# Optimization experiments

Measured on AMD Instinct MI355X. Metric: run time of the kernel, lower is better.

Reference implementation:

```python
import jax, jax.numpy as jnp
import numpy as np

B, S, R = 8, 4096, 512
E, K, ATOMS, XAR, TOPK = 64, 256, 16, 3, 2
TEMP = 1.0


def setup_inputs() -> dict:
    key = jax.random.key(0)
    k0, k1, k2, k3, k4 = jax.random.split(key, 5)
    x_latent = jax.random.normal(k0, (B, S, R), jnp.float32)
    router_w = jax.random.normal(k1, (E, R), jnp.float32) * (1.0 / np.sqrt(R))
    atoms = jax.random.normal(k2, (E, ATOMS, R), jnp.float32) * 0.01
    combo_weights = jax.random.uniform(k3, (E, K, XAR), jnp.float32) * 0.5 + 0.25
    combo_logits = jax.random.normal(k4, (E, K, XAR, ATOMS), jnp.float32) * 0.01
    return {"x_latent": x_latent, "router_w": router_w, "atoms": atoms,
            "combo_weights": combo_weights, "combo_logits": combo_logits}


def _expert_centroids(atoms, combo_weights, combo_logits):
    # Hard codeword path (vectorized over experts):
    # sign atoms -> pick argmax atom per (k, xor slot) -> weight -> sum -> sign -> mean over k
    binary = jnp.sign(atoms)                                   # [E, A, R]
    # softmax(logits/t) then argmax == argmax(logits) (monotone)
    idx = jnp.argmax(combo_logits, axis=-1)                    # [E, K, XAR]
    sel = binary[jnp.arange(E)[:, None, None], idx]            # [E, K, XAR, R]
    codewords = jnp.sign((sel * combo_weights[..., None]).sum(axis=2))  # [E, K, R]
    return codewords.mean(axis=1)                              # [E, R]


def reference(x_latent, router_w, atoms, combo_weights, combo_logits):
    t = max(TEMP, 0.1)
    router_logits = jnp.einsum('bsr,er->bse', x_latent, router_w)   # [B, S, E]
    probs_t = jax.nn.softmax(router_logits / t, axis=-1)
    gates, expert_ids = jax.lax.top_k(probs_t, TOPK)                # [B, S, 2]
    gates = gates / gates.sum(axis=-1, keepdims=True)

    centroids = _expert_centroids(atoms, combo_weights, combo_logits)  # [E, R]

    # aux load-balancing loss (uses untempered softmax)
    router_prob = jax.nn.softmax(router_logits, axis=-1)
    aux_loss = E * jnp.sum(router_prob.mean(axis=(0, 1)) *
                           (router_prob > 0).astype(x_latent.dtype).mean(axis=(0, 1)))

    # dense per-expert gate = sum over topk slots of gate * (id == e), then combine with centroids
    dense_gates = (jax.nn.one_hot(expert_ids, E, dtype=gates.dtype) *
                   gates[..., None]).sum(axis=-2)                    # [B, S, E]
    combined = jnp.einsum('bse,er->bsr', dense_gates, centroids)     # [B, S, R]
    return combined, aux_loss
```

## Files before the change

### kernel.cpp

```cpp
#include <hip/hip_runtime.h>
#include <math.h>

#define TOKENS 32768
#define RDIM 512
#define NEXP 64
#define NK 256
#define LDB 264
#define PSTR 67
#define TAU 4.0e-3f

typedef unsigned short u16;
typedef float f32x4 __attribute__((ext_vector_type(4)));
typedef short s16x8 __attribute__((ext_vector_type(8)));

#define MFMA_B16(a, b, c) __builtin_amdgcn_mfma_f32_16x16x32_bf16(a, b, c, 0, 0, 0)

__device__ __forceinline__ void split_pack(float4 v, unsigned& h01, unsigned& h23,
                                           unsigned& l01, unsigned& l23) {
    unsigned u0 = __float_as_uint(v.x), u1 = __float_as_uint(v.y);
    unsigned u2 = __float_as_uint(v.z), u3 = __float_as_uint(v.w);
    float r0 = v.x - __uint_as_float(u0 & 0xFFFF0000u);
    float r1 = v.y - __uint_as_float(u1 & 0xFFFF0000u);
    float r2 = v.z - __uint_as_float(u2 & 0xFFFF0000u);
    float r3 = v.w - __uint_as_float(u3 & 0xFFFF0000u);
    h01 = (u0 >> 16) | (u1 & 0xFFFF0000u);
    h23 = (u2 >> 16) | (u3 & 0xFFFF0000u);
    l01 = (__float_as_uint(r0) >> 16) | (__float_as_uint(r1) & 0xFFFF0000u);
    l23 = (__float_as_uint(r2) >> 16) | (__float_as_uint(r3) & 0xFFFF0000u);
}

__device__ __forceinline__ void split8(float4 a, float4 b, s16x8& hi, s16x8& lo) {
    union U { unsigned u[4]; s16x8 v; };
    U H, L;
    split_pack(a, H.u[0], H.u[1], L.u[0], L.u[1]);
    split_pack(b, H.u[2], H.u[3], L.u[2], L.u[3]);
    hi = H.v; lo = L.v;
}

__global__ __launch_bounds__(256) void centroid_kernel(
    const float* __restrict__ atoms,
    const float* __restrict__ cw,
    const float* __restrict__ cl,
    float* __restrict__ cent,
    float* __restrict__ aux_sum,
    unsigned* __restrict__ aux_cnt,
    unsigned* __restrict__ done)
{
    __shared__ unsigned pack[NK];
    const int e    = blockIdx.x >> 1;
    const int half = blockIdx.x & 1;
    const int tid  = threadIdx.x;

    if (blockIdx.x == 0 && tid < 64) { aux_sum[tid] = 0.f; aux_cnt[tid] = 0u; }
    if (done && blockIdx.x == 0 && tid == 0) *done = 0u;

    {
        const int k = tid;
        unsigned u = 0;
        float w3[3];
        #pragma unroll
        for (int xx = 0; xx < 3; ++xx) {
            const float* cp = cl + ((((size_t)e * NK + k) * 3 + xx) << 4);
            float v[16];
            *(float4*)(v + 0)  = *(const float4*)(cp + 0);
            *(float4*)(v + 4)  = *(const float4*)(cp + 4);
            *(float4*)(v + 8)  = *(const float4*)(cp + 8);
            *(float4*)(v + 12) = *(const float4*)(cp + 12);
            float best = v[0]; int bi = 0;
            #pragma unroll
            for (int a = 1; a < 16; ++a) {
                if (v[a] > best) { best = v[a]; bi = a; }
            }
            u |= (unsigned)bi << (4 * xx);
            w3[xx] = cw[((size_t)e * NK + k) * 3 + xx];
        }
        unsigned lut = 0;
        #pragma unroll
        for (int c = 0; c < 8; ++c) {
            float val = ((c & 1) ? -w3[0] : w3[0])
                      + ((c & 2) ? -w3[1] : w3[1])
                      + ((c & 4) ? -w3[2] : w3[2]);
            lut |= (val < 0.f ? 1u : 0u) << c;
        }
        pack[k] = u | (lut << 16);
    }

    const int r = half * 256 + tid;
    unsigned B0 = 0;
    #pragma unroll
    for (int a = 0; a < 16; ++a)
        B0 |= (atoms[((size_t)e * 16 + a) * RDIM + r] < 0.f ? 1u : 0u) << a;
    __syncthreads();

    int n0 = 0;
    for (int k = 0; k < NK; ++k) {
        unsigned u  = pack[k];
        unsigned i0 = u & 15u, i1 = (u >> 4) & 15u, i2 = (u >> 8) & 15u;
        unsigned c0 = ((B0 >> i0) & 1u) | (((B0 >> i1) & 1u) << 1) | (((B0 >> i2) & 1u) << 2);
        n0 += (u >> (16 + c0)) & 1u;
    }
    cent[(size_t)e * RDIM + r] = 1.f - (float)n0 * (1.f / 128.f);
}

__global__ __launch_bounds__(512, 2) void moe_main(
    const float* __restrict__ x,
    const float* __restrict__ w,
    const float* __restrict__ cent,
    float* __restrict__ out,
    float* __restrict__ aux_sum,
    unsigned* __restrict__ aux_cnt,
    unsigned* __restrict__ done,
    float* __restrict__ out_aux,
    int fuse)
{
    __shared__ u16 wlds[2 * 64 * LDB];
    u16* whi = wlds;
    u16* wlo = wlds + 64 * LDB;
    float* P     = (float*)wlds;
    float* candv = P + 128 * PSTR;
    int*   candi = (int*)(candv + 128 * 13);
    float* qsum  = (float*)(candi + 128 * 13);
    float* gateL = qsum + 128 * 5;
    __shared__ float s_aux[64];
    __shared__ unsigned s_cnt[64];
    __shared__ int s_last;

    const int tid  = threadIdx.x;
    const int lane = tid & 63;
    const int wave = tid >> 6;
    const int l15  = lane & 15;
    const int kgrp = (lane >> 4) << 3;
    const int tok0 = blockIdx.x * 128;

    if (tid < 64) { s_aux[tid] = 0.f; s_cnt[tid] = 0u; }

    f32x4 acc[4];
    #pragma unroll
    for (int nt = 0; nt < 4; ++nt) acc[nt] = (f32x4){0.f, 0.f, 0.f, 0.f};

    const float* xlane = x + (size_t)(tok0 + wave * 16 + l15) * RDIM + kgrp;
    const int wrow = tid >> 3;
    const int wseg = tid & 7;
    const float* wg = w + (size_t)wrow * RDIM + wseg * 32;
    const int woff = wrow * LDB + wseg * 32;

    float4 wpre[8];
    #pragma unroll
    for (int j = 0; j < 8; ++j) wpre[j] = *(const float4*)(wg + j * 4);

    float4 preA[4], preB[4];
    #pragma unroll
    for (int i = 0; i < 4; ++i) {
        preA[i] = *(const float4*)(xlane + i * 32);
        preB[i] = *(const float4*)(xlane + i * 32 + 4);
    }

    #pragma unroll
    for (int h = 0; h < 2; ++h) {
        if (h) __syncthreads();
        #pragma unroll
        for (int j = 0; j < 8; ++j) {
            unsigned h01, h23, l01, l23;
            split_pack(wpre[j], h01, h23, l01, l23);
            *(uint2*)&whi[woff + j * 4] = make_uint2(h01, h23);
            *(uint2*)&wlo[woff + j * 4] = make_uint2(l01, l23);
        }
        __syncthreads();

        #pragma unroll
        for (int kb = 0; kb < 8; ++kb) {
            s16x8 ah, al;
            split8(preA[kb & 3], preB[kb & 3], ah, al);
            const int gk = h * 8 + kb + 4;
            if (gk < 16) {
                const float* nx = xlane + gk * 32;
                preA[kb & 3] = *(const float4*)(nx);
                preB[kb & 3] = *(const float4*)(nx + 4);
            }
            if (h == 0 && kb == 2) {
                #pragma unroll
                for (int j = 0; j < 8; ++j)
                    wpre[j] = *(const float4*)(wg + 256 + j * 4);
            }
            const int kl = kb * 32 + kgrp;
            #pragma unroll
            for (int nt = 0; nt < 4; ++nt) {
                const int brow = nt * 16 + l15;
                s16x8 bh = *(const s16x8*)&whi[brow * LDB + kl];
                s16x8 bl = *(const s16x8*)&wlo[brow * LDB + kl];
                acc[nt] = MFMA_B16(ah, bh, acc[nt]);
                acc[nt] = MFMA_B16(ah, bl, acc[nt]);
                acc[nt] = MFMA_B16(al, bh, acc[nt]);
            }
        }
    }

    __syncthreads();
    #pragma unroll
    for (int nt = 0; nt < 4; ++nt)
        #pragma unroll
        for (int i = 0; i < 4; ++i)
            P[(wave * 16 + ((lane >> 4) << 2) + i) * PSTR + nt * 16 + l15] = acc[nt][i];
    __syncthreads();

    const int tt = tid & 127;
    const int ss = tid >> 7;
    float v[16];
    #pragma unroll
    for (int j = 0; j < 16; ++j) v[j] = P[tt * PSTR + ss * 16 + j];

    float m1 = -INFINITY, m2 = -INFINITY, m3 = -INFINITY;
    int   i1 = NEXP, i2 = NEXP, i3 = NEXP;
    #pragma unroll
    for (int j = 0; j < 16; ++j) {
        float val = v[j]; int e = ss * 16 + j;
        if (val > m1)      { m3 = m2; i3 = i2; m2 = m1; i2 = i1; m1 = val; i1 = e; }
        else if (val > m2) { m3 = m2; i3 = i2; m2 = val; i2 = e; }
        else if (val > m3) { m3 = val; i3 = e; }
    }
    candv[tt * 13 + ss * 3 + 0] = m1; candi[tt * 13 + ss * 3 + 0] = i1;
    candv[tt * 13 + ss * 3 + 1] = m2; candi[tt * 13 + ss * 3 + 1] = i2;
    candv[tt * 13 + ss * 3 + 2] = m3; candi[tt * 13 + ss * 3 + 2] = i3;
    __syncthreads();

    m1 = m2 = m3 = -INFINITY; i1 = i2 = i3 = NEXP;
    #pragma unroll
    for (int q = 0; q < 12; ++q) {
        float val = candv[tt * 13 + q]; int e = candi[tt * 13 + q];
        if (val > m1)      { m3 = m2; i3 = i2; m2 = m1; i2 = i1; m1 = val; i1 = e; }
        else if (val > m2) { m3 = m2; i3 = i2; m2 = val; i2 = e; }
        else if (val > m3) { m3 = val; i3 = e; }
    }

    float ex[16]; float ps = 0.f;
    #pragma unroll
    for (int j = 0; j < 16; ++j) { ex[j] = __expf(v[j] - m1); ps += ex[j]; }
    qsum[tt * 5 + ss] = ps;

    if (ss == 0) {
        {
            const float ed  = __expf(m2 - m1);
            const float inv = 1.f / (1.f + ed);
            gateL[tt * 4 + 0] = inv;
            gateL[tt * 4 + 1] = ed * inv;
            ((int*)gateL)[tt * 4 + 2] = i1;
            ((int*)gateL)[tt * 4 + 3] = i2;
        }
        const int tbase = wave << 6;
        unsigned long long bmask = __ballot(m2 - m3 < TAU);
        while (bmask) {
            const int f = __ffsll(bmask) - 1;
            bmask &= bmask - 1;
            int id3[3];
            id3[0] = __shfl(i1, f); id3[1] = __shfl(i2, f); id3[2] = __shfl(i3, f);
            const float* xrow = x + (size_t)(tok0 + tbase + f) * RDIM + lane * 8;
            float4 a0 = *(const float4*)(xrow);
            float4 a1 = *(const float4*)(xrow + 4);
            float d[3];
            #pragma unroll
            for (int jj = 0; jj < 3; ++jj) {
                const float* wrow = w + (size_t)id3[jj] * RDIM + lane * 8;
                float4 b0 = *(const float4*)(wrow);
                float4 b1 = *(const float4*)(wrow + 4);
                float p = a0.x * b0.x;
                p = fmaf(a0.y, b0.y, p); p = fmaf(a0.z, b0.z, p); p = fmaf(a0.w, b0.w, p);
                p = fmaf(a1.x, b1.x, p); p = fmaf(a1.y, b1.y, p);
                p = fmaf(a1.z, b1.z, p); p = fmaf(a1.w, b1.w, p);
                #pragma unroll
                for (int off = 32; off; off >>= 1) p += __shfl_xor(p, off);
                d[jj] = p;
            }
            int b = 0;
            if (d[1] > d[0] || (d[1] == d[0] && id3[1] < id3[0])) b = 1;
            if (d[2] > d[b] || (d[2] == d[b] && id3[2] < id3[b])) b = 2;
            int sec;
            if (b == 0)      sec = (d[1] > d[2] || (d[1] == d[2] && id3[1] < id3[2])) ? 1 : 2;
            else if (b == 1) sec = (d[0] > d[2] || (d[0] == d[2] && id3[0] < id3[2])) ? 0 : 2;
            else             sec = (d[0] > d[1] || (d[0] == d[1] && id3[0] < id3[1])) ? 0 : 1;
            if (lane == f) {
                const float ed  = __expf(d[sec] - d[b]);
                const float inv = 1.f / (1.f + ed);
                gateL[(tbase + f) * 4 + 0] = inv;
                gateL[(tbase + f) * 4 + 1] = ed * inv;
                ((int*)gateL)[(tbase + f) * 4 + 2] = id3[b];
                ((int*)gateL)[(tbase + f) * 4 + 3] = id3[sec];
            }
        }
    }
    __syncthreads();

    float Z = 0.f;
    #pragma unroll
    for (int k = 0; k < 4; ++k) Z += qsum[tt * 5 + k];
    const float invZ = 1.f / Z;
    #pragma unroll
    for (int j = 0; j < 16; ++j) P[tt * PSTR + ss * 16 + j] = ex[j] * invZ;
    __syncthreads();

    {
        const int e = tid & 63, tq = tid >> 6;
        float s = 0.f; unsigned cn = 0u;
        #pragma unroll
        for (int t = 0; t < 16; ++t) {
            float pv = P[(tq * 16 + t) * PSTR + e];
            s += pv; cn += (pv > 0.f) ? 1u : 0u;
        }
        atomicAdd(&s_aux[e], s);
        atomicAdd(&s_cnt[e], cn);
    }
    __syncthreads();
    if (tid < 64) {
        atomicAdd(aux_sum + tid, s_aux[tid]);
        atomicAdd(aux_cnt + tid, s_cnt[tid]);
    }

    {
        const int e = lane;
        #pragma unroll
        for (int s2 = 0; s2 < 16; ++s2) {
            const int t2 = wave * 16 + s2;
            float4 g4 = *(float4*)&gateL[t2 * 4];
            const float g1 = g4.x, g2 = g4.y;
            const int e1 = __float_as_int(g4.z), e2 = __float_as_int(g4.w);
            const float4* c1 = (const float4*)(cent + (size_t)e1 * RDIM);
            const float4* c2 = (const float4*)(cent + (size_t)e2 * RDIM);
            float4* op = (float4*)(out + (size_t)(tok0 + t2) * RDIM);
            float4 A0 = c1[e],      Bb0 = c2[e];
            float4 A1 = c1[e + 64], Bb1 = c2[e + 64];
            float4 o0, o1;
            o0.x = fmaf(g1, A0.x, g2 * Bb0.x); o0.y = fmaf(g1, A0.y, g2 * Bb0.y);
            o0.z = fmaf(g1, A0.z, g2 * Bb0.z); o0.w = fmaf(g1, A0.w, g2 * Bb0.w);
            o1.x = fmaf(g1, A1.x, g2 * Bb1.x); o1.y = fmaf(g1, A1.y, g2 * Bb1.y);
            o1.z = fmaf(g1, A1.z, g2 * Bb1.z); o1.w = fmaf(g1, A1.w, g2 * Bb1.w);
            op[e]      = o0;
            op[e + 64] = o1;
        }
    }

    if (fuse) {
        __syncthreads();
        if (tid == 0) {
            __threadfence();
            s_last = (atomicAdd(done, 1u) == 255u) ? 1 : 0;
        }
        __syncthreads();
        if (s_last && tid < 64) {
            float    sv = atomicAdd(&aux_sum[tid], 0.f);
            unsigned cv = atomicAdd(&aux_cnt[tid], 0u);
            float val = (sv * (1.f / (float)TOKENS)) * ((float)cv * (1.f / (float)TOKENS));
            #pragma unroll
            for (int off = 32; off; off >>= 1) val += __shfl_xor(val, off);
            if (tid == 0) out_aux[0] = (float)NEXP * val;
        }
    }
}

__global__ __launch_bounds__(64) void aux_kernel(
    const float* __restrict__ sums,
    const unsigned* __restrict__ cnts,
    float* __restrict__ out_aux)
{
    const int e = threadIdx.x;
    float v = (sums[e] * (1.f / (float)TOKENS)) * ((float)cnts[e] * (1.f / (float)TOKENS));
    #pragma unroll
    for (int off = 32; off; off >>= 1) v += __shfl_xor(v, off);
    if (e == 0) out_aux[0] = (float)NEXP * v;
}

extern "C" void kernel_launch(void* const* d_in, const int* in_sizes, int n_in,
                              void* d_out, int out_size, void* d_ws, size_t ws_size,
                              hipStream_t stream) {
    const float* x     = (const float*)d_in[0];
    const float* rw    = (const float*)d_in[1];
    const float* atoms = (const float*)d_in[2];
    const float* cwts  = (const float*)d_in[3];
    const float* clog  = (const float*)d_in[4];
    float* out = (float*)d_out;

    const bool fused = ws_size >= (size_t)(1024 + NEXP * RDIM * 4);
    float*    aux_sum = (float*)d_ws;
    unsigned* aux_cnt = (unsigned*)((char*)d_ws + 256);
    unsigned* done    = fused ? (unsigned*)((char*)d_ws + 512) : nullptr;
    float*    cent    = (float*)((char*)d_ws + (fused ? 1024 : 512));

    centroid_kernel<<<128, 256, 0, stream>>>(atoms, cwts, clog, cent, aux_sum, aux_cnt, done);
    moe_main<<<256, 512, 0, stream>>>(x, rw, cent, out, aux_sum, aux_cnt, done,
                                      out + (size_t)TOKENS * RDIM, fused ? 1 : 0);
    if (!fused)
        aux_kernel<<<1, 64, 0, stream>>>(aux_sum, aux_cnt, out + (size_t)TOKENS * RDIM);
}
```

Measured before the change: 163.0 us.

## Shrink main blocks to 64 tokens, stage router weights in quarters, drop fused aux

moe_main now uses 256-thread blocks over 64 tokens, with 512 blocks and launch bounds allowing 4 blocks per CU. It stages the router weight in four 128-column quarters instead of two halves, which shrinks LDS use and drops the register prefetch of weights. The last-block atomic fusion of the aux loss is removed in favour of always launching the separate aux kernel, and the centroid inner loop is batched 8 at a time. The aim is higher occupancy and lower LDS and register pressure. The cost is more barriers, more reloads of the weight matrix per token, and an extra kernel launch.

```diff
diff --git a/kernel.cpp b/kernel.cpp
--- a/kernel.cpp
+++ b/kernel.cpp
@@ -5,7 +5,7 @@
 #define RDIM 512
 #define NEXP 64
 #define NK 256
-#define LDB 264
+#define LDQ 136
 #define PSTR 67
 #define TAU 4.0e-3f
 
@@ -43,8 +43,7 @@
     const float* __restrict__ cl,
     float* __restrict__ cent,
     float* __restrict__ aux_sum,
-    unsigned* __restrict__ aux_cnt,
-    unsigned* __restrict__ done)
+    unsigned* __restrict__ aux_cnt)
 {
     __shared__ unsigned pack[NK];
     const int e    = blockIdx.x >> 1;
@@ -52,7 +51,6 @@
     const int tid  = threadIdx.x;
 
     if (blockIdx.x == 0 && tid < 64) { aux_sum[tid] = 0.f; aux_cnt[tid] = 0u; }
-    if (done && blockIdx.x == 0 && tid == 0) *done = 0u;
 
     {
         const int k = tid;
@@ -93,44 +91,47 @@
     __syncthreads();
 
     int n0 = 0;
-    for (int k = 0; k < NK; ++k) {
-        unsigned u  = pack[k];
-        unsigned i0 = u & 15u, i1 = (u >> 4) & 15u, i2 = (u >> 8) & 15u;
-        unsigned c0 = ((B0 >> i0) & 1u) | (((B0 >> i1) & 1u) << 1) | (((B0 >> i2) & 1u) << 2);
-        n0 += (u >> (16 + c0)) & 1u;
+    #pragma unroll 2
+    for (int k = 0; k < NK; k += 8) {
+        unsigned pk[8];
+        #pragma unroll
+        for (int j = 0; j < 8; ++j) pk[j] = pack[k + j];
+        #pragma unroll
+        for (int j = 0; j < 8; ++j) {
+            unsigned u  = pk[j];
+            unsigned i0 = u & 15u, i1 = (u >> 4) & 15u, i2 = (u >> 8) & 15u;
+            unsigned c0 = ((B0 >> i0) & 1u) | (((B0 >> i1) & 1u) << 1) | (((B0 >> i2) & 1u) << 2);
+            n0 += (u >> (16 + c0)) & 1u;
+        }
     }
     cent[(size_t)e * RDIM + r] = 1.f - (float)n0 * (1.f / 128.f);
 }
 
-__global__ __launch_bounds__(512, 2) void moe_main(
+__global__ __launch_bounds__(256, 4) void moe_main(
     const float* __restrict__ x,
     const float* __restrict__ w,
     const float* __restrict__ cent,
     float* __restrict__ out,
     float* __restrict__ aux_sum,
-    unsigned* __restrict__ aux_cnt,
-    unsigned* __restrict__ done,
-    float* __restrict__ out_aux,
-    int fuse)
+    unsigned* __restrict__ aux_cnt)
 {
-    __shared__ u16 wlds[2 * 64 * LDB];
+    __shared__ u16 wlds[2 * 64 * LDQ];
     u16* whi = wlds;
-    u16* wlo = wlds + 64 * LDB;
+    u16* wlo = wlds + 64 * LDQ;
     float* P     = (float*)wlds;
-    float* candv = P + 128 * PSTR;
-    int*   candi = (int*)(candv + 128 * 13);
-    float* qsum  = (float*)(candi + 128 * 13);
-    float* gateL = qsum + 128 * 5;
+    float* candv = P + 64 * PSTR;
+    int*   candi = (int*)(candv + 64 * 13);
+    float* qsum  = (float*)(candi + 64 * 13);
+    float* gateL = qsum + 64 * 5;
     __shared__ float s_aux[64];
     __shared__ unsigned s_cnt[64];
-    __shared__ int s_last;
 
     const int tid  = threadIdx.x;
     const int lane = tid & 63;
     const int wave = tid >> 6;
     const int l15  = lane & 15;
     const int kgrp = (lane >> 4) << 3;
-    const int tok0 = blockIdx.x * 128;
+    const int tok0 = blockIdx.x * 64;
 
     if (tid < 64) { s_aux[tid] = 0.f; s_cnt[tid] = 0u; }
 
@@ -139,14 +140,10 @@
     for (int nt = 0; nt < 4; ++nt) acc[nt] = (f32x4){0.f, 0.f, 0.f, 0.f};
 
     const float* xlane = x + (size_t)(tok0 + wave * 16 + l15) * RDIM + kgrp;
-    const int wrow = tid >> 3;
-    const int wseg = tid & 7;
+    const int wrow = tid >> 2;
+    const int wseg = tid & 3;
     const float* wg = w + (size_t)wrow * RDIM + wseg * 32;
-    const int woff = wrow * LDB + wseg * 32;
-
-    float4 wpre[8];
-    #pragma unroll
-    for (int j = 0; j < 8; ++j) wpre[j] = *(const float4*)(wg + j * 4);
+    const int woff = wrow * LDQ + wseg * 32;
 
     float4 preA[4], preB[4];
     #pragma unroll
@@ -156,38 +153,41 @@
     }
 
     #pragma unroll
-    for (int h = 0; h < 2; ++h) {
-        if (h) __syncthreads();
-        #pragma unroll
-        for (int j = 0; j < 8; ++j) {
-            unsigned h01, h23, l01, l23;
-            split_pack(wpre[j], h01, h23, l01, l23);
-            *(uint2*)&whi[woff + j * 4] = make_uint2(h01, h23);
-            *(uint2*)&wlo[woff + j * 4] = make_uint2(l01, l23);
+    for (int q = 0; q < 4; ++q) {
+        if (q) __syncthreads();
+        {
+            const float* wq = wg + q * 128;
+            uint2 h2[2], l2[2];
+            #pragma unroll
+            for (int j = 0; j < 8; ++j) {
+                float4 wv = *(const float4*)(wq + j * 4);
+                split_pack(wv, h2[j & 1].x, h2[j & 1].y, l2[j & 1].x, l2[j & 1].y);
+                if (j & 1) {
+                    *(uint4*)&whi[woff + (j - 1) * 4] =
+                        make_uint4(h2[0].x, h2[0].y, h2[1].x, h2[1].y);
+                    *(uint4*)&wlo[woff + (j - 1) * 4] =
+                        make_uint4(l2[0].x, l2[0].y, l2[1].x, l2[1].y);
+                }
+            }
         }
         __syncthreads();
 
         #pragma unroll
-        for (int kb = 0; kb < 8; ++kb) {
+        for (int kb = 0; kb < 4; ++kb) {
+            const int g = q * 4 + kb;
             s16x8 ah, al;
-            split8(preA[kb & 3], preB[kb & 3], ah, al);
-            const int gk = h * 8 + kb + 4;
-            if (gk < 16) {
-                const float* nx = xlane + gk * 32;
-                preA[kb & 3] = *(const float4*)(nx);
-                preB[kb & 3] = *(const float4*)(nx + 4);
-            }
-            if (h == 0 && kb == 2) {
-                #pragma unroll
-                for (int j = 0; j < 8; ++j)
-                    wpre[j] = *(const float4*)(wg + 256 + j * 4);
+            split8(preA[g & 3], preB[g & 3], ah, al);
+            if (g + 4 < 16) {
+                const float* nx = xlane + (g + 4) * 32;
+                preA[g & 3] = *(const float4*)(nx);
+                preB[g & 3] = *(const float4*)(nx + 4);
             }
             const int kl = kb * 32 + kgrp;
             #pragma unroll
             for (int nt = 0; nt < 4; ++nt) {
                 const int brow = nt * 16 + l15;
-                s16x8 bh = *(const s16x8*)&whi[brow * LDB + kl];
-                s16x8 bl = *(const s16x8*)&wlo[brow * LDB + kl];
+                s16x8 bh = *(const s16x8*)&whi[brow * LDQ + kl];
+                s16x8 bl = *(const s16x8*)&wlo[brow * LDQ + kl];
                 acc[nt] = MFMA_B16(ah, bh, acc[nt]);
                 acc[nt] = MFMA_B16(ah, bl, acc[nt]);
                 acc[nt] = MFMA_B16(al, bh, acc[nt]);
@@ -203,8 +203,8 @@
             P[(wave * 16 + ((lane >> 4) << 2) + i) * PSTR + nt * 16 + l15] = acc[nt][i];
     __syncthreads();
 
-    const int tt = tid & 127;
-    const int ss = tid >> 7;
+    const int tt = tid & 63;
+    const int ss = tid >> 6;
     float v[16];
     #pragma unroll
     for (int j = 0; j < 16; ++j) v[j] = P[tt * PSTR + ss * 16 + j];
@@ -246,22 +246,21 @@
             ((int*)gateL)[tt * 4 + 2] = i1;
             ((int*)gateL)[tt * 4 + 3] = i2;
         }
-        const int tbase = wave << 6;
         unsigned long long bmask = __ballot(m2 - m3 < TAU);
         while (bmask) {
             const int f = __ffsll(bmask) - 1;
             bmask &= bmask - 1;
             int id3[3];
             id3[0] = __shfl(i1, f); id3[1] = __shfl(i2, f); id3[2] = __shfl(i3, f);
-            const float* xrow = x + (size_t)(tok0 + tbase + f) * RDIM + lane * 8;
+            const float* xrow = x + (size_t)(tok0 + f) * RDIM + lane * 8;
             float4 a0 = *(const float4*)(xrow);
             float4 a1 = *(const float4*)(xrow + 4);
             float d[3];
             #pragma unroll
             for (int jj = 0; jj < 3; ++jj) {
-                const float* wrow = w + (size_t)id3[jj] * RDIM + lane * 8;
-                float4 b0 = *(const float4*)(wrow);
-                float4 b1 = *(const float4*)(wrow + 4);
+                const float* wrow2 = w + (size_t)id3[jj] * RDIM + lane * 8;
+                float4 b0 = *(const float4*)(wrow2);
+                float4 b1 = *(const float4*)(wrow2 + 4);
                 float p = a0.x * b0.x;
                 p = fmaf(a0.y, b0.y, p); p = fmaf(a0.z, b0.z, p); p = fmaf(a0.w, b0.w, p);
                 p = fmaf(a1.x, b1.x, p); p = fmaf(a1.y, b1.y, p);
@@ -280,10 +279,10 @@
             if (lane == f) {
                 const float ed  = __expf(d[sec] - d[b]);
                 const float inv = 1.f / (1.f + ed);
-                gateL[(tbase + f) * 4 + 0] = inv;
-                gateL[(tbase + f) * 4 + 1] = ed * inv;
-                ((int*)gateL)[(tbase + f) * 4 + 2] = id3[b];
-                ((int*)gateL)[(tbase + f) * 4 + 3] = id3[sec];
+                gateL[f * 4 + 0] = inv;
+                gateL[f * 4 + 1] = ed * inv;
+                ((int*)gateL)[f * 4 + 2] = id3[b];
+                ((int*)gateL)[f * 4 + 3] = id3[sec];
             }
         }
     }
@@ -336,23 +335,6 @@
             op[e + 64] = o1;
         }
     }
-
-    if (fuse) {
-        __syncthreads();
-        if (tid == 0) {
-            __threadfence();
-            s_last = (atomicAdd(done, 1u) == 255u) ? 1 : 0;
-        }
-        __syncthreads();
-        if (s_last && tid < 64) {
-            float    sv = atomicAdd(&aux_sum[tid], 0.f);
-            unsigned cv = atomicAdd(&aux_cnt[tid], 0u);
-            float val = (sv * (1.f / (float)TOKENS)) * ((float)cv * (1.f / (float)TOKENS));
-            #pragma unroll
-            for (int off = 32; off; off >>= 1) val += __shfl_xor(val, off);
-            if (tid == 0) out_aux[0] = (float)NEXP * val;
-        }
-    }
 }
 
 __global__ __launch_bounds__(64) void aux_kernel(
@@ -377,15 +359,11 @@
     const float* clog  = (const float*)d_in[4];
     float* out = (float*)d_out;
 
-    const bool fused = ws_size >= (size_t)(1024 + NEXP * RDIM * 4);
     float*    aux_sum = (float*)d_ws;
     unsigned* aux_cnt = (unsigned*)((char*)d_ws + 256);
-    unsigned* done    = fused ? (unsigned*)((char*)d_ws + 512) : nullptr;
-    float*    cent    = (float*)((char*)d_ws + (fused ? 1024 : 512));
-
-    centroid_kernel<<<128, 256, 0, stream>>>(atoms, cwts, clog, cent, aux_sum, aux_cnt, done);
-    moe_main<<<256, 512, 0, stream>>>(x, rw, cent, out, aux_sum, aux_cnt, done,
-                                      out + (size_t)TOKENS * RDIM, fused ? 1 : 0);
-    if (!fused)
-        aux_kernel<<<1, 64, 0, stream>>>(aux_sum, aux_cnt, out + (size_t)TOKENS * RDIM);
-}
+    float*    cent    = (float*)((char*)d_ws + 512);
+
+    centroid_kernel<<<128, 256, 0, stream>>>(atoms, cwts, clog, cent, aux_sum, aux_cnt);
+    moe_main<<<512, 256, 0, stream>>>(x, rw, cent, out, aux_sum, aux_cnt);
+    aux_kernel<<<1, 64, 0, stream>>>(aux_sum, aux_cnt, out + (size_t)TOKENS * RDIM);
+}
```

Measured after the change: 165.7 us. About the same (+1.7%).
